# Kernel optimization log

Hardware: AMD Instinct MI355X
Metric: run time of the kernel (lower is better)

Reference implementation:

```python
import jax, jax.numpy as jnp
import numpy as np

DIM = 64  # number of flow dimensions (block count)


def _masks(out_f, in_f, dim):
    # mask_d: 1 on the dim diagonal blocks; mask_o: 1 strictly below-block (lower-triangular off-diagonal)
    opd, ipd = out_f // dim, in_f // dim
    mask_d = np.zeros((out_f, in_f), np.float32)
    mask_o = np.ones((out_f, in_f), np.float32)
    for i in range(dim):
        mask_d[i * opd:(i + 1) * opd, i * ipd:(i + 1) * ipd] = 1.0
        mask_o[i * opd:(i + 1) * opd, i * ipd:] = 0.0
    return jnp.asarray(mask_d), jnp.asarray(mask_o)


def setup_inputs() -> dict:
    key = jax.random.key(0)
    k1, k2, k3, k4, k5 = jax.random.split(key, 5)
    B, F = 1024, 2048
    inputs = jax.random.normal(k1, (B, F), jnp.float32)
    # log-diagonal Jacobian blocks from a previous layer with per-dim input size 1
    grad = jax.random.normal(k2, (B, DIM, F // DIM, 1), jnp.float32)
    weight = jax.random.normal(k3, (F, F), jnp.float32) * 0.05
    diag_weight = jnp.log(jax.random.uniform(k4, (F, 1), jnp.float32, 1e-3, 1.0))
    bias = jax.random.uniform(k5, (F,), jnp.float32, -1.0, 1.0) / jnp.sqrt(jnp.float32(F))
    return {"inputs": inputs, "grad": grad, "weight": weight,
            "diag_weight": diag_weight, "bias": bias}


def reference(inputs, grad, weight, diag_weight, bias):
    out_f, in_f = weight.shape
    dim = DIM
    opd, ipd = out_f // dim, in_f // dim
    mask_d, mask_o = _masks(out_f, in_f, dim)

    # weight normalization with positive diagonal blocks
    w = jnp.exp(weight) * mask_d + weight * mask_o              # (out, in)
    wsn = jnp.sum(w * w, axis=-1, keepdims=True)                # (out, 1)
    w_n = jnp.exp(diag_weight) * w / jnp.sqrt(wsn)              # (out, in)
    wpl = diag_weight + weight - 0.5 * jnp.log(wsn)             # (out, in)

    out = inputs @ w_n.T + bias                                 # (B, out)

    # diagonal blocks of wpl, already transposed per-block: (dim, opd, ipd)
    wpl4 = wpl.reshape(dim, opd, dim, ipd)
    blocks = wpl4[jnp.arange(dim), :, jnp.arange(dim), :]

    B = inputs.shape[0]
    g = jnp.broadcast_to(blocks[None], (B, dim, opd, ipd))

    # combine with previous log-Jacobian: logsumexp over contracted axis
    grad_t = jnp.swapaxes(grad, -1, -2)                         # (B, dim, p, ipd)
    logdet = jax.nn.logsumexp(g[:, :, :, None, :] + grad_t[:, :, None, :, :], axis=-1)  # (B, dim, opd, p)
    return (out, logdet)
```

## Files before the change

### kernel.cpp

```cpp
#include <hip/hip_runtime.h>

#define F 2048
#define BATCH 1024

typedef short bf16x8 __attribute__((ext_vector_type(8)));
typedef float f32x4 __attribute__((ext_vector_type(4)));

__device__ __forceinline__ unsigned short f2bf(float f) {
  unsigned u = __builtin_bit_cast(unsigned, f);
  unsigned r = (u + 0x7fffu + ((u >> 16) & 1u)) >> 16;
  return (unsigned short)r;
}

__device__ __forceinline__ void gload_lds16(const void* g, void* l) {
  __builtin_amdgcn_global_load_lds(
      (const __attribute__((address_space(1))) unsigned int*)g,
      (__attribute__((address_space(3))) unsigned int*)l,
      16, 0, 0);
}

__global__ __launch_bounds__(256) void convert_kernel(
    const float* __restrict__ in, unsigned short* __restrict__ out)
{
  int idx = (blockIdx.x * 256 + threadIdx.x) * 8;
  float4 v0 = *(const float4*)(in + idx);
  float4 v1 = *(const float4*)(in + idx + 4);
  union { unsigned short s[8]; bf16x8 v; } o;
  o.s[0] = f2bf(v0.x); o.s[1] = f2bf(v0.y); o.s[2] = f2bf(v0.z); o.s[3] = f2bf(v0.w);
  o.s[4] = f2bf(v1.x); o.s[5] = f2bf(v1.y); o.s[6] = f2bf(v1.z); o.s[7] = f2bf(v1.w);
  *(bf16x8*)(out + idx) = o.v;
}

__global__ __launch_bounds__(256) void prep_kernel(
    const float* __restrict__ weight, const float* __restrict__ dw,
    unsigned short* __restrict__ w_n, float* __restrict__ exp_blocks)
{
  int r = blockIdx.x;
  int i = r >> 5;
  int lim = (i + 1) * 32;
  int wlim = (r & ~63) + 64;
  int tid = threadIdx.x;
  const float* wrow = weight + (size_t)r * F;

  float ss = 0.f;
  for (int c = tid; c < lim; c += 256) {
    float wv = wrow[c];
    float w = (c >= i * 32) ? __expf(wv) : wv;
    ss += w * w;
  }
  __shared__ float red[256];
  red[tid] = ss;
  __syncthreads();
  for (int s = 128; s > 0; s >>= 1) {
    if (tid < s) red[tid] += red[tid + s];
    __syncthreads();
  }
  float wsn = red[0];
  float dwr = dw[r];
  float scale = __expf(dwr) * rsqrtf(wsn);
  float halflog = 0.5f * __logf(wsn);

  unsigned short* onrow = w_n + (size_t)r * F;
  for (int c = tid; c < wlim; c += 256) {
    float v = 0.f;
    if (c < lim) {
      float wv = wrow[c];
      v = scale * ((c >= i * 32) ? __expf(wv) : wv);
    }
    onrow[c] = f2bf(v);
  }
  if (tid < 32) {
    float wv = wrow[i * 32 + tid];
    exp_blocks[(size_t)r * 32 + tid] = __expf(dwr + wv - halflog);
  }
}

__global__ __launch_bounds__(256) void gemm_kernel(
    const unsigned short* __restrict__ A, const unsigned short* __restrict__ W,
    const float* __restrict__ bias, float* __restrict__ out)
{
  __shared__ char smem[2][2][8192];

  int id = blockIdx.x;
  int tm = id >> 5;
  int tn_raw = id & 31;
  int tn = (tm & 8) ? (31 - tn_raw) : tn_raw;
  int m0 = tm * 64, n0 = tn * 64;
  int nkt = tn + 1;

  int tid = threadIdx.x;
  int lane = tid & 63, wid = tid >> 6;
  int wm = wid >> 1, wn = wid & 1;
  int l15 = lane & 15, lg = lane >> 4;

  int srow = lane >> 3;
  int schunk = (lane & 7) ^ (srow & 7);

  auto stage = [&](int buf, int kt) {
    size_t kb = (size_t)kt * 128;
#pragma unroll
    for (int e = 0; e < 2; ++e) {
      int s = wid * 2 + e;
      int row = s * 8 + srow;
      const char* ga = (const char*)A + (size_t)(m0 + row) * (F * 2) + kb + schunk * 16;
      gload_lds16(ga, &smem[buf][0][s * 1024]);
      const char* gb = (const char*)W + (size_t)(n0 + row) * (F * 2) + kb + schunk * 16;
      gload_lds16(gb, &smem[buf][1][s * 1024]);
    }
  };

  f32x4 acc[2][2] = {};

  auto compute = [&](int buf) {
    const char* sA = smem[buf][0];
    const char* sB = smem[buf][1];
    bf16x8 af[2][2], bfr[2][2];
#pragma unroll
    for (int mi = 0; mi < 2; ++mi)
#pragma unroll
      for (int ks = 0; ks < 2; ++ks) {
        int row = wm * 32 + mi * 16 + l15;
        int ch = (ks * 4 + lg) ^ (l15 & 7);
        af[mi][ks] = *(const bf16x8*)(sA + row * 128 + ch * 16);
      }
#pragma unroll
    for (int ni = 0; ni < 2; ++ni)
#pragma unroll
      for (int ks = 0; ks < 2; ++ks) {
        int row = wn * 32 + ni * 16 + l15;
        int ch = (ks * 4 + lg) ^ (l15 & 7);
        bfr[ni][ks] = *(const bf16x8*)(sB + row * 128 + ch * 16);
      }
#pragma unroll
    for (int ks = 0; ks < 2; ++ks)
#pragma unroll
      for (int mi = 0; mi < 2; ++mi)
#pragma unroll
        for (int ni = 0; ni < 2; ++ni)
          acc[mi][ni] = __builtin_amdgcn_mfma_f32_16x16x32_bf16(
              af[mi][ks], bfr[ni][ks], acc[mi][ni], 0, 0, 0);
  };

  stage(0, 0);
  __syncthreads();
  int cur = 0;
  for (int kt = 0; kt < nkt; ++kt) {
    if (kt + 1 < nkt) stage(cur ^ 1, kt + 1);
    compute(cur);
    __syncthreads();
    cur ^= 1;
  }

  float bv0 = bias[n0 + wn * 32 + l15];
  float bv1 = bias[n0 + wn * 32 + 16 + l15];
#pragma unroll
  for (int mi = 0; mi < 2; ++mi)
#pragma unroll
    for (int ni = 0; ni < 2; ++ni) {
      float bv = ni ? bv1 : bv0;
#pragma unroll
      for (int j = 0; j < 4; ++j) {
        int m = m0 + wm * 32 + mi * 16 + lg * 4 + j;
        int n = n0 + wn * 32 + ni * 16 + l15;
        out[(size_t)m * F + n] = acc[mi][ni][j] + bv;
      }
    }
}

__global__ __launch_bounds__(256) void logdet_kernel(
    const float* __restrict__ grad, const float* __restrict__ exp_blocks,
    float* __restrict__ ld)
{
  __shared__ float eb[32][33];
  __shared__ float eg[8][32];
  int i = blockIdx.x & 63;
  int bg = blockIdx.x >> 6;
  int tid = threadIdx.x;
  for (int t = tid; t < 1024; t += 256) {
    eb[t >> 5][t & 31] = exp_blocks[(size_t)i * 1024 + t];
  }
  int pair = tid >> 5, p = tid & 31;
  int b = bg * 8 + pair;
  eg[pair][p] = __expf(grad[((size_t)b * 64 + i) * 32 + p]);
  __syncthreads();
  int o = p;
  float s = 0.f;
#pragma unroll
  for (int q = 0; q < 32; ++q) s += eb[o][q] * eg[pair][q];
  ld[((size_t)b * 64 + i) * 32 + o] = __logf(s);
}

extern "C" void kernel_launch(void* const* d_in, const int* in_sizes, int n_in,
                              void* d_out, int out_size, void* d_ws, size_t ws_size,
                              hipStream_t stream)
{
  const float* inputs = (const float*)d_in[0];
  const float* grad   = (const float*)d_in[1];
  const float* weight = (const float*)d_in[2];
  const float* dw     = (const float*)d_in[3];
  const float* bias   = (const float*)d_in[4];

  float* out = (float*)d_out;
  float* ld  = out + (size_t)BATCH * F;

  unsigned short* w_n  = (unsigned short*)d_ws;
  unsigned short* a_bf = w_n + (size_t)F * F;
  float* exp_blocks    = (float*)(a_bf + (size_t)BATCH * F);

  convert_kernel<<<BATCH * F / 2048, 256, 0, stream>>>(inputs, a_bf);
  prep_kernel<<<F, 256, 0, stream>>>(weight, dw, w_n, exp_blocks);
  gemm_kernel<<<512, 256, 0, stream>>>(a_bf, w_n, bias, out);
  logdet_kernel<<<64 * 128, 256, 0, stream>>>(grad, exp_blocks, ld);
}
```

Before: 120.3 us.

## Fuse convert and prep kernels, triple-buffer GEMM, widen logdet per block

The input bf16 conversion and the weight-normalization prep now run in one launch. Prep uses one wavefront per row with float4 loads and shuffle reductions in place of a shared-memory tree with block barriers. The GEMM moves from double to triple-buffered LDS staging with explicit vmcnt waits, so global loads run further ahead of compute. The logdet kernel handles 32 batch rows per block, reusing each exp-block element across four accumulators and cutting the grid size, at the cost of more LDS and registers per block.

```diff
diff --git a/kernel.cpp b/kernel.cpp
--- a/kernel.cpp
+++ b/kernel.cpp
@@ -5,6 +5,7 @@
 
 typedef short bf16x8 __attribute__((ext_vector_type(8)));
 typedef float f32x4 __attribute__((ext_vector_type(4)));
+typedef unsigned short u16x4 __attribute__((ext_vector_type(4)));
 
 __device__ __forceinline__ unsigned short f2bf(float f) {
   unsigned u = __builtin_bit_cast(unsigned, f);
@@ -19,59 +20,61 @@
       16, 0, 0);
 }
 
-__global__ __launch_bounds__(256) void convert_kernel(
-    const float* __restrict__ in, unsigned short* __restrict__ out)
-{
-  int idx = (blockIdx.x * 256 + threadIdx.x) * 8;
-  float4 v0 = *(const float4*)(in + idx);
-  float4 v1 = *(const float4*)(in + idx + 4);
-  union { unsigned short s[8]; bf16x8 v; } o;
-  o.s[0] = f2bf(v0.x); o.s[1] = f2bf(v0.y); o.s[2] = f2bf(v0.z); o.s[3] = f2bf(v0.w);
-  o.s[4] = f2bf(v1.x); o.s[5] = f2bf(v1.y); o.s[6] = f2bf(v1.z); o.s[7] = f2bf(v1.w);
-  *(bf16x8*)(out + idx) = o.v;
-}
-
-__global__ __launch_bounds__(256) void prep_kernel(
+__global__ __launch_bounds__(256) void prep_convert_kernel(
+    const float* __restrict__ inputs, unsigned short* __restrict__ a_bf,
     const float* __restrict__ weight, const float* __restrict__ dw,
     unsigned short* __restrict__ w_n, float* __restrict__ exp_blocks)
 {
-  int r = blockIdx.x;
+  int bid = blockIdx.x;
+  if (bid < 1024) {
+    int idx = bid * 2048 + threadIdx.x * 8;
+    float4 v0 = *(const float4*)(inputs + idx);
+    float4 v1 = *(const float4*)(inputs + idx + 4);
+    union { unsigned short s[8]; bf16x8 v; } o;
+    o.s[0] = f2bf(v0.x); o.s[1] = f2bf(v0.y); o.s[2] = f2bf(v0.z); o.s[3] = f2bf(v0.w);
+    o.s[4] = f2bf(v1.x); o.s[5] = f2bf(v1.y); o.s[6] = f2bf(v1.z); o.s[7] = f2bf(v1.w);
+    *(bf16x8*)(a_bf + idx) = o.v;
+    return;
+  }
+  int rb = bid - 1024;
+  int lane = threadIdx.x & 63;
+  int r = rb * 4 + (threadIdx.x >> 6);
   int i = r >> 5;
   int lim = (i + 1) * 32;
   int wlim = (r & ~63) + 64;
-  int tid = threadIdx.x;
+  int d0 = i * 32;
   const float* wrow = weight + (size_t)r * F;
 
   float ss = 0.f;
-  for (int c = tid; c < lim; c += 256) {
-    float wv = wrow[c];
-    float w = (c >= i * 32) ? __expf(wv) : wv;
-    ss += w * w;
-  }
-  __shared__ float red[256];
-  red[tid] = ss;
-  __syncthreads();
-  for (int s = 128; s > 0; s >>= 1) {
-    if (tid < s) red[tid] += red[tid + s];
-    __syncthreads();
-  }
-  float wsn = red[0];
+  for (int j = lane; j < lim / 4; j += 64) {
+    float4 v = ((const float4*)wrow)[j];
+    if (j * 4 >= d0) {
+      v.x = __expf(v.x); v.y = __expf(v.y); v.z = __expf(v.z); v.w = __expf(v.w);
+    }
+    ss += v.x * v.x + v.y * v.y + v.z * v.z + v.w * v.w;
+  }
+#pragma unroll
+  for (int d = 32; d > 0; d >>= 1) ss += __shfl_xor(ss, d, 64);
+
   float dwr = dw[r];
-  float scale = __expf(dwr) * rsqrtf(wsn);
-  float halflog = 0.5f * __logf(wsn);
+  float scale = __expf(dwr) * rsqrtf(ss);
+  float halflog = 0.5f * __logf(ss);
 
   unsigned short* onrow = w_n + (size_t)r * F;
-  for (int c = tid; c < wlim; c += 256) {
-    float v = 0.f;
-    if (c < lim) {
-      float wv = wrow[c];
-      v = scale * ((c >= i * 32) ? __expf(wv) : wv);
-    }
-    onrow[c] = f2bf(v);
-  }
-  if (tid < 32) {
-    float wv = wrow[i * 32 + tid];
-    exp_blocks[(size_t)r * 32 + tid] = __expf(dwr + wv - halflog);
+  for (int j = lane; j < wlim / 4; j += 64) {
+    u16x4 o = {0, 0, 0, 0};
+    if (j * 4 < lim) {
+      float4 v = ((const float4*)wrow)[j];
+      if (j * 4 >= d0) {
+        v.x = __expf(v.x); v.y = __expf(v.y); v.z = __expf(v.z); v.w = __expf(v.w);
+      }
+      o[0] = f2bf(scale * v.x); o[1] = f2bf(scale * v.y);
+      o[2] = f2bf(scale * v.z); o[3] = f2bf(scale * v.w);
+    }
+    *(u16x4*)(onrow + j * 4) = o;
+  }
+  if (lane < 32) {
+    exp_blocks[(size_t)r * 32 + lane] = __expf(dwr + wrow[d0 + lane] - halflog);
   }
 }
 
@@ -79,7 +82,7 @@
     const unsigned short* __restrict__ A, const unsigned short* __restrict__ W,
     const float* __restrict__ bias, float* __restrict__ out)
 {
-  __shared__ char smem[2][2][8192];
+  __shared__ char smem[3][2][8192];
 
   int id = blockIdx.x;
   int tm = id >> 5;
@@ -142,13 +145,16 @@
   };
 
   stage(0, 0);
-  __syncthreads();
-  int cur = 0;
+  if (nkt > 1) stage(1, 1);
   for (int kt = 0; kt < nkt; ++kt) {
-    if (kt + 1 < nkt) stage(cur ^ 1, kt + 1);
-    compute(cur);
-    __syncthreads();
-    cur ^= 1;
+    if (kt + 2 < nkt) stage((kt + 2) % 3, kt + 2);
+    int rem = nkt - 1 - kt;
+    if (rem >= 2)      asm volatile("s_waitcnt vmcnt(8)" ::: "memory");
+    else if (rem == 1) asm volatile("s_waitcnt vmcnt(4)" ::: "memory");
+    else               asm volatile("s_waitcnt vmcnt(0)" ::: "memory");
+    __builtin_amdgcn_s_barrier();
+    compute(kt % 3);
+    __builtin_amdgcn_s_barrier();
   }
 
   float bv0 = bias[n0 + wn * 32 + l15];
@@ -172,22 +178,37 @@
     float* __restrict__ ld)
 {
   __shared__ float eb[32][33];
-  __shared__ float eg[8][32];
+  __shared__ float eg[32][32];
   int i = blockIdx.x & 63;
-  int bg = blockIdx.x >> 6;
+  int b0 = (blockIdx.x >> 6) * 32;
   int tid = threadIdx.x;
-  for (int t = tid; t < 1024; t += 256) {
+  int p = tid & 31, row8 = tid >> 5;
+
+#pragma unroll
+  for (int k = 0; k < 4; ++k) {
+    int t = tid + k * 256;
     eb[t >> 5][t & 31] = exp_blocks[(size_t)i * 1024 + t];
   }
-  int pair = tid >> 5, p = tid & 31;
-  int b = bg * 8 + pair;
-  eg[pair][p] = __expf(grad[((size_t)b * 64 + i) * 32 + p]);
+#pragma unroll
+  for (int k = 0; k < 4; ++k) {
+    int b = b0 + row8 + 8 * k;
+    eg[row8 + 8 * k][p] = __expf(grad[((size_t)b * 64 + i) * 32 + p]);
+  }
   __syncthreads();
+
   int o = p;
-  float s = 0.f;
-#pragma unroll
-  for (int q = 0; q < 32; ++q) s += eb[o][q] * eg[pair][q];
-  ld[((size_t)b * 64 + i) * 32 + o] = __logf(s);
+  float s[4] = {0.f, 0.f, 0.f, 0.f};
+#pragma unroll
+  for (int q = 0; q < 32; ++q) {
+    float e = eb[o][q];
+#pragma unroll
+    for (int k = 0; k < 4; ++k) s[k] += e * eg[row8 + 8 * k][q];
+  }
+#pragma unroll
+  for (int k = 0; k < 4; ++k) {
+    int b = b0 + row8 + 8 * k;
+    ld[((size_t)b * 64 + i) * 32 + o] = __logf(s[k]);
+  }
 }
 
 extern "C" void kernel_launch(void* const* d_in, const int* in_sizes, int n_in,
@@ -207,8 +228,7 @@
   unsigned short* a_bf = w_n + (size_t)F * F;
   float* exp_blocks    = (float*)(a_bf + (size_t)BATCH * F);
 
-  convert_kernel<<<BATCH * F / 2048, 256, 0, stream>>>(inputs, a_bf);
-  prep_kernel<<<F, 256, 0, stream>>>(weight, dw, w_n, exp_blocks);
+  prep_convert_kernel<<<1536, 256, 0, stream>>>(inputs, a_bf, weight, dw, w_n, exp_blocks);
   gemm_kernel<<<512, 256, 0, stream>>>(a_bf, w_n, bias, out);
-  logdet_kernel<<<64 * 128, 256, 0, stream>>>(grad, exp_blocks, ld);
-}
+  logdet_kernel<<<64 * 32, 256, 0, stream>>>(grad, exp_blocks, ld);
+}
```

New measurement: 106.6 us. 1.13x faster.
